# Performance work log

Hardware: AMD Instinct MI355X
Metric: run time of the kernel (lower is better)

The kernel has to match this reference:

```python
import jax, jax.numpy as jnp
import numpy as np

B, L, C, K, F = 32, 8192, 128, 7, 128


def setup_inputs() -> dict:
    key = jax.random.key(0)
    kx, kw = jax.random.split(key)
    x = jax.random.normal(kx, (B, L, C, 1), dtype=jnp.float32)
    # glorot-style scale for the learned kernel [K, C, F]
    scale = jnp.sqrt(2.0 / (K * C + F)).astype(jnp.float32)
    kernel = jax.random.normal(kw, (K, C, F), dtype=jnp.float32) * scale
    return {"x": x, "kernel": kernel}


def reference(x, kernel):
    # x: [B, L, C, 1]; kernel: [K, C, F]
    # Original loop computes out[b,i,f] = sum_{k,c} x[b,i+k,c,0] * kernel[k,c,f]
    # which is a valid-padding 1D convolution.
    xs = x[..., 0]  # [B, L, C]
    out = jax.lax.conv_general_dilated(
        xs, kernel,
        window_strides=(1,),
        padding="VALID",
        dimension_numbers=("NWC", "WIO", "NWC"),
    )  # [B, L-K+1, F]
    return out[..., None]  # [B, L-K+1, F, 1]
```

## Files before the change

kernel.cpp:

```cpp
#include <hip/hip_runtime.h>
#include <hip/hip_bf16.h>

#define BATCH 32
#define LEN   8192
#define CDIM  128
#define TAPS  7
#define FDIM  128
#define LOUT  (LEN - TAPS + 1)
#define BM    128
#define XROWS (BM + TAPS - 1)

typedef __attribute__((ext_vector_type(8)))  short bf16x8;
typedef __attribute__((ext_vector_type(16))) float f32x16;

#if defined(__has_builtin)
#  if __has_builtin(__builtin_amdgcn_global_load_lds)
#    define USE_GLL 1
#  endif
#endif
#ifndef USE_GLL
#  define USE_GLL 0
#endif

static __device__ __forceinline__ unsigned short bf16_rne(float f) {
    unsigned u = __float_as_uint(f);
    u += 0x7FFFu + ((u >> 16) & 1u);
    return (unsigned short)(u >> 16);
}
static __device__ __forceinline__ unsigned pack2(float a, float b) {
    return (unsigned)bf16_rne(a) | ((unsigned)bf16_rne(b) << 16);
}

__global__ void wconv_kernel(const float* __restrict__ w, ushort* __restrict__ wt) {
    int idx = blockIdx.x * 256 + threadIdx.x;
    int k = idx >> 14;
    int rem = idx & 16383;
    int f = rem >> 7;
    int c = rem & 127;
    wt[idx] = bf16_rne(w[(k << 14) + (c << 7) + f]);
}

__global__ __launch_bounds__(256, 2)
void conv_gemm_kernel(const float* __restrict__ x, const ushort* __restrict__ wt,
                      float* __restrict__ out) {
    __shared__ __align__(16) ushort Xs[XROWS * CDIM];
    __shared__ __align__(16) ushort Ws[FDIM * CDIM];

    const int tid  = threadIdx.x;
    const int lane = tid & 63;
    const int wid  = tid >> 6;
    const int wm   = wid >> 1;
    const int wn   = wid & 1;
    const int l31  = lane & 31;
    const int l5   = lane >> 5;

    const int bid  = blockIdx.x;
    const int b    = bid >> 6;
    const int i0   = (bid & 63) * BM;

    const float* xb = x + (size_t)b * LEN * CDIM;

    for (int q = tid; q < XROWS * 16; q += 256) {
        int r   = q >> 4;
        int col = q & 15;
        int gi  = i0 + r;
        float4 v0, v1;
        if (gi < LEN) {
            const float4* p = (const float4*)(xb + (size_t)gi * CDIM + col * 8);
            v0 = p[0]; v1 = p[1];
        } else {
            v0 = make_float4(0.f, 0.f, 0.f, 0.f);
            v1 = v0;
        }
        int scol = col ^ (r & 15);
        uint4 pk;
        pk.x = pack2(v0.x, v0.y);
        pk.y = pack2(v0.z, v0.w);
        pk.z = pack2(v1.x, v1.y);
        pk.w = pack2(v1.z, v1.w);
        *(uint4*)&Xs[r * CDIM + scol * 8] = pk;
    }

    auto stage_w = [&](int t) {
#if USE_GLL
        const ushort* wt_t = wt + t * (FDIM * CDIM);
        #pragma unroll
        for (int it = 0; it < 8; ++it) {
            int cidx = it * 256 + tid;
            int f  = cidx >> 4;
            int j  = cidx & 15;
            int sj = j ^ (f & 15);
            const ushort* g = wt_t + f * CDIM + sj * 8;
            ushort* l = &Ws[(it * 256 + (tid & 192)) * 8];
            __builtin_amdgcn_global_load_lds(
                (const __attribute__((address_space(1))) void*)g,
                (__attribute__((address_space(3))) void*)l, 16, 0, 0);
        }
#else
        const ushort* wt_t = wt + t * (FDIM * CDIM);
        #pragma unroll
        for (int it = 0; it < 8; ++it) {
            int cidx = it * 256 + tid;
            int f  = cidx >> 4;
            int j  = cidx & 15;
            int sj = j ^ (f & 15);
            uint4 v = *(const uint4*)(wt_t + f * CDIM + sj * 8);
            *(uint4*)&Ws[cidx * 8] = v;
        }
#endif
    };

    stage_w(0);
    __syncthreads();

    f32x16 acc[2][2] = {};

    #pragma unroll
    for (int t = 0; t < TAPS; ++t) {
        const int r0 = (wm << 6) + l31 + t;
        const int r1 = r0 + 32;
        const int f0 = (wn << 6) + l31;
        const int f1 = f0 + 32;
        #pragma unroll
        for (int kk = 0; kk < 8; ++kk) {
            int j = kk * 2 + l5;
            bf16x8 a0 = *(const bf16x8*)&Xs[r0 * CDIM + ((j ^ (r0 & 15)) << 3)];
            bf16x8 a1 = *(const bf16x8*)&Xs[r1 * CDIM + ((j ^ (r1 & 15)) << 3)];
            bf16x8 b0 = *(const bf16x8*)&Ws[f0 * CDIM + ((j ^ (f0 & 15)) << 3)];
            bf16x8 b1 = *(const bf16x8*)&Ws[f1 * CDIM + ((j ^ (f1 & 15)) << 3)];
            acc[0][0] = __builtin_amdgcn_mfma_f32_32x32x16_bf16(a0, b0, acc[0][0], 0, 0, 0);
            acc[0][1] = __builtin_amdgcn_mfma_f32_32x32x16_bf16(a0, b1, acc[0][1], 0, 0, 0);
            acc[1][0] = __builtin_amdgcn_mfma_f32_32x32x16_bf16(a1, b0, acc[1][0], 0, 0, 0);
            acc[1][1] = __builtin_amdgcn_mfma_f32_32x32x16_bf16(a1, b1, acc[1][1], 0, 0, 0);
        }
        if (t < TAPS - 1) {
            __syncthreads();
            stage_w(t + 1);
            __syncthreads();
        }
    }

    float* ob = out + (size_t)b * LOUT * FDIM;
    #pragma unroll
    for (int fm = 0; fm < 2; ++fm) {
        #pragma unroll
        for (int fn = 0; fn < 2; ++fn) {
            #pragma unroll
            for (int r = 0; r < 16; ++r) {
                int row = (wm << 6) + (fm << 5) + (r & 3) + ((r >> 2) << 3) + (l5 << 2);
                int i = i0 + row;
                if (i < LOUT) {
                    ob[(size_t)i * FDIM + (wn << 6) + (fn << 5) + l31] = acc[fm][fn][r];
                }
            }
        }
    }
}

extern "C" void kernel_launch(void* const* d_in, const int* in_sizes, int n_in,
                              void* d_out, int out_size, void* d_ws, size_t ws_size,
                              hipStream_t stream) {
    const float* x = (const float*)d_in[0];
    const float* w = (const float*)d_in[1];
    float* out = (float*)d_out;
    ushort* wt = (ushort*)d_ws;

    wconv_kernel<<<448, 256, 0, stream>>>(w, wt);
    conv_gemm_kernel<<<BATCH * 64, 256, 0, stream>>>(x, wt, out);
}
```

Baseline: 273.0 us.

## Load weight fragments directly from global into registers, drop LDS weight staging

Removes the shared-memory buffer for the weight tile and the per-tap barrier-bracketed staging. Each wave now loads its B fragments for a tap straight from global memory (L2-cached bf16 weights) into registers before the MFMA loop. With LDS usage cut to the input tile, launch bounds are raised to three blocks per CU. The aim is to remove the twelve barriers and LDS traffic per block. The cost is extra global and L2 load traffic, since every block rereads the weights, and higher register pressure from 16 fragment vectors.

```diff
diff --git a/kernel.cpp b/kernel.cpp
--- a/kernel.cpp
+++ b/kernel.cpp
@@ -12,15 +12,6 @@
 
 typedef __attribute__((ext_vector_type(8)))  short bf16x8;
 typedef __attribute__((ext_vector_type(16))) float f32x16;
-
-#if defined(__has_builtin)
-#  if __has_builtin(__builtin_amdgcn_global_load_lds)
-#    define USE_GLL 1
-#  endif
-#endif
-#ifndef USE_GLL
-#  define USE_GLL 0
-#endif
 
 static __device__ __forceinline__ unsigned short bf16_rne(float f) {
     unsigned u = __float_as_uint(f);
@@ -40,11 +31,10 @@
     wt[idx] = bf16_rne(w[(k << 14) + (c << 7) + f]);
 }
 
-__global__ __launch_bounds__(256, 2)
+__global__ __launch_bounds__(256, 3)
 void conv_gemm_kernel(const float* __restrict__ x, const ushort* __restrict__ wt,
                       float* __restrict__ out) {
     __shared__ __align__(16) ushort Xs[XROWS * CDIM];
-    __shared__ __align__(16) ushort Ws[FDIM * CDIM];
 
     const int tid  = threadIdx.x;
     const int lane = tid & 63;
@@ -60,83 +50,61 @@
 
     const float* xb = x + (size_t)b * LEN * CDIM;
 
-    for (int q = tid; q < XROWS * 16; q += 256) {
-        int r   = q >> 4;
-        int col = q & 15;
-        int gi  = i0 + r;
-        float4 v0, v1;
-        if (gi < LEN) {
-            const float4* p = (const float4*)(xb + (size_t)gi * CDIM + col * 8);
-            v0 = p[0]; v1 = p[1];
-        } else {
-            v0 = make_float4(0.f, 0.f, 0.f, 0.f);
-            v1 = v0;
+    #pragma unroll
+    for (int it = 0; it < 9; ++it) {
+        int q = it * 256 + tid;
+        if (q < XROWS * 16) {
+            int r   = q >> 4;
+            int col = q & 15;
+            int gi  = i0 + r;
+            float4 v0, v1;
+            if (gi < LEN) {
+                const float4* p = (const float4*)(xb + (size_t)gi * CDIM + col * 8);
+                v0 = p[0]; v1 = p[1];
+            } else {
+                v0 = make_float4(0.f, 0.f, 0.f, 0.f);
+                v1 = v0;
+            }
+            int scol = col ^ (r & 15);
+            uint4 pk;
+            pk.x = pack2(v0.x, v0.y);
+            pk.y = pack2(v0.z, v0.w);
+            pk.z = pack2(v1.x, v1.y);
+            pk.w = pack2(v1.z, v1.w);
+            *(uint4*)&Xs[r * CDIM + scol * 8] = pk;
         }
-        int scol = col ^ (r & 15);
-        uint4 pk;
-        pk.x = pack2(v0.x, v0.y);
-        pk.y = pack2(v0.z, v0.w);
-        pk.z = pack2(v1.x, v1.y);
-        pk.w = pack2(v1.z, v1.w);
-        *(uint4*)&Xs[r * CDIM + scol * 8] = pk;
     }
 
-    auto stage_w = [&](int t) {
-#if USE_GLL
-        const ushort* wt_t = wt + t * (FDIM * CDIM);
-        #pragma unroll
-        for (int it = 0; it < 8; ++it) {
-            int cidx = it * 256 + tid;
-            int f  = cidx >> 4;
-            int j  = cidx & 15;
-            int sj = j ^ (f & 15);
-            const ushort* g = wt_t + f * CDIM + sj * 8;
-            ushort* l = &Ws[(it * 256 + (tid & 192)) * 8];
-            __builtin_amdgcn_global_load_lds(
-                (const __attribute__((address_space(1))) void*)g,
-                (__attribute__((address_space(3))) void*)l, 16, 0, 0);
-        }
-#else
-        const ushort* wt_t = wt + t * (FDIM * CDIM);
-        #pragma unroll
-        for (int it = 0; it < 8; ++it) {
-            int cidx = it * 256 + tid;
-            int f  = cidx >> 4;
-            int j  = cidx & 15;
-            int sj = j ^ (f & 15);
-            uint4 v = *(const uint4*)(wt_t + f * CDIM + sj * 8);
-            *(uint4*)&Ws[cidx * 8] = v;
-        }
-#endif
-    };
-
-    stage_w(0);
     __syncthreads();
 
     f32x16 acc[2][2] = {};
 
+    const int f0 = (wn << 6) + l31;
+    const int f1 = f0 + 32;
+
     #pragma unroll
     for (int t = 0; t < TAPS; ++t) {
+        const ushort* wt_t = wt + t * (FDIM * CDIM);
         const int r0 = (wm << 6) + l31 + t;
         const int r1 = r0 + 32;
-        const int f0 = (wn << 6) + l31;
-        const int f1 = f0 + 32;
+
+        bf16x8 b0[8], b1[8];
+        #pragma unroll
+        for (int kk = 0; kk < 8; ++kk) {
+            int off = (kk * 2 + l5) << 3;
+            b0[kk] = *(const bf16x8*)(wt_t + f0 * CDIM + off);
+            b1[kk] = *(const bf16x8*)(wt_t + f1 * CDIM + off);
+        }
+
         #pragma unroll
         for (int kk = 0; kk < 8; ++kk) {
             int j = kk * 2 + l5;
             bf16x8 a0 = *(const bf16x8*)&Xs[r0 * CDIM + ((j ^ (r0 & 15)) << 3)];
             bf16x8 a1 = *(const bf16x8*)&Xs[r1 * CDIM + ((j ^ (r1 & 15)) << 3)];
-            bf16x8 b0 = *(const bf16x8*)&Ws[f0 * CDIM + ((j ^ (f0 & 15)) << 3)];
-            bf16x8 b1 = *(const bf16x8*)&Ws[f1 * CDIM + ((j ^ (f1 & 15)) << 3)];
-            acc[0][0] = __builtin_amdgcn_mfma_f32_32x32x16_bf16(a0, b0, acc[0][0], 0, 0, 0);
-            acc[0][1] = __builtin_amdgcn_mfma_f32_32x32x16_bf16(a0, b1, acc[0][1], 0, 0, 0);
-            acc[1][0] = __builtin_amdgcn_mfma_f32_32x32x16_bf16(a1, b0, acc[1][0], 0, 0, 0);
-            acc[1][1] = __builtin_amdgcn_mfma_f32_32x32x16_bf16(a1, b1, acc[1][1], 0, 0, 0);
-        }
-        if (t < TAPS - 1) {
-            __syncthreads();
-            stage_w(t + 1);
-            __syncthreads();
+            acc[0][0] = __builtin_amdgcn_mfma_f32_32x32x16_bf16(a0, b0[kk], acc[0][0], 0, 0, 0);
+            acc[0][1] = __builtin_amdgcn_mfma_f32_32x32x16_bf16(a0, b1[kk], acc[0][1], 0, 0, 0);
+            acc[1][0] = __builtin_amdgcn_mfma_f32_32x32x16_bf16(a1, b0[kk], acc[1][0], 0, 0, 0);
+            acc[1][1] = __builtin_amdgcn_mfma_f32_32x32x16_bf16(a1, b1[kk], acc[1][1], 0, 0, 0);
         }
     }
 
```

Result: slower. 327.4 us (+20.0%).
